# Optimization experiments

Measured on AMD Instinct MI355X. Metric: run time of the kernel, lower is better.

The kernel has to match this reference:

```python
import jax, jax.numpy as jnp
import numpy as np

# wav2vec2 feature-extractor conv stack config: (kernel, stride) per layer, 512 channels
CONV_CFG = [(10, 5), (3, 2), (3, 2), (3, 2), (3, 2), (2, 2), (2, 2)]
C = 512
PROJ = 256
HID = 128
NCLS = 5
N_WORDS = 64
B = 8
L = 40000


def _conv1d(h, w, stride):
    # h: [B, Cin, T], w: [Cout, Cin, K]
    return jax.lax.conv_general_dilated(
        h, w, window_strides=(stride,), padding='VALID',
        dimension_numbers=('NCH', 'OIH', 'NCH'))


def setup_inputs() -> dict:
    key = jax.random.key(0)
    ks = jax.random.split(key, 16)
    x = jax.random.normal(ks[0], (B, L), dtype=jnp.float32)
    word_ids = jax.random.randint(ks[1], (B,), 0, N_WORDS)
    convs = {}
    cin = 1
    for i, (k, s) in enumerate(CONV_CFG):
        fan = cin * k
        convs[f'conv{i}'] = jax.random.normal(ks[2 + i], (C, cin, k), dtype=jnp.float32) / np.sqrt(fan)
        cin = C
    gn_scale = jnp.ones((C,), dtype=jnp.float32)
    gn_bias = jnp.zeros((C,), dtype=jnp.float32)
    proj_w = jax.random.normal(ks[9], (PROJ, C), dtype=jnp.float32) / np.sqrt(C)
    proj_b = jnp.zeros((PROJ,), dtype=jnp.float32)
    cls_w1 = jax.random.normal(ks[10], (N_WORDS, PROJ, HID), dtype=jnp.float32) / np.sqrt(PROJ)
    cls_b1 = jnp.zeros((N_WORDS, HID), dtype=jnp.float32)
    cls_w2 = jax.random.normal(ks[11], (N_WORDS, HID, NCLS), dtype=jnp.float32) / np.sqrt(HID)
    cls_b2 = jnp.zeros((N_WORDS, NCLS), dtype=jnp.float32)
    return dict(x=x, word_ids=word_ids, gn_scale=gn_scale, gn_bias=gn_bias,
                proj_w=proj_w, proj_b=proj_b, cls_w1=cls_w1, cls_b1=cls_b1,
                cls_w2=cls_w2, cls_b2=cls_b2, **convs)


def _forward(x, convs, gn_scale, gn_bias, proj_w, proj_b, cls_w1, cls_b1, cls_w2, cls_b2, word_ids):
    h = x[:, None, :]  # [B,1,L]
    for i, (k, s) in enumerate(CONV_CFG):
        h = _conv1d(h, convs[i], s)
        if i == 0:
            # wav2vec2 group-norm: groups == channels -> per-channel norm over time
            mu = jnp.mean(h, axis=-1, keepdims=True)
            var = jnp.var(h, axis=-1, keepdims=True)
            h = (h - mu) * jax.lax.rsqrt(var + 1e-5)
            h = h * gn_scale[None, :, None] + gn_bias[None, :, None]
        h = jax.nn.gelu(h)
    feat = jnp.mean(h, axis=-1)                          # [B, 512] mean-pool over time
    feat = jax.nn.relu(feat @ proj_w.T + proj_b)         # [B, 256] (dropout = identity in eval)
    w1 = cls_w1[word_ids]                                # [B, 256, 128] routed gather
    h1 = jax.nn.relu(jnp.einsum('bd,bdh->bh', feat, w1) + cls_b1[word_ids])
    out = jnp.einsum('bh,bho->bo', h1, cls_w2[word_ids]) + cls_b2[word_ids]  # [B, 5]
    return out


def reference(x, word_ids, gn_scale, gn_bias, proj_w, proj_b, cls_w1, cls_b1, cls_w2, cls_b2,
              conv0, conv1, conv2, conv3, conv4, conv5, conv6):
    convs = [conv0, conv1, conv2, conv3, conv4, conv5, conv6]
    return _forward(x, convs, gn_scale, gn_bias, proj_w, proj_b,
                    cls_w1, cls_b1, cls_w2, cls_b2, word_ids)
```

## Files before the change

kernel.cpp:

```cpp
#include <hip/hip_runtime.h>
#include <hip/hip_bf16.h>

typedef unsigned short u16;
typedef short bf16x8 __attribute__((ext_vector_type(8)));
typedef float f32x4 __attribute__((ext_vector_type(4)));

#define CC 512

constexpr int vmimm(int n) {
    return (n & 0xF) | ((n >> 4) << 14) | (0x7 << 4) | (0xF << 8);
}

__device__ __forceinline__ float gelu_tanh(float x) {
    float x3 = x * x * x;
    float z  = 0.7978845608028654f * (x + 0.044715f * x3);
    float e  = __expf(2.0f * z);
    float th = 1.0f - 2.0f / (e + 1.0f);
    return 0.5f * x * (1.0f + th);
}

__device__ __forceinline__ u16 f2bf(float f) {
    union { float f; unsigned u; } v; v.f = f;
    unsigned r = v.u + 0x7fff + ((v.u >> 16) & 1);
    return (u16)(r >> 16);
}
__device__ __forceinline__ float bf2f(u16 h) {
    union { unsigned u; float f; } v; v.u = ((unsigned)h) << 16; return v.f;
}

__global__ __launch_bounds__(256) void conv0_store(
    const float* __restrict__ x, const float* __restrict__ w0,
    u16* __restrict__ actG, float* __restrict__ part) {
    const int t0 = blockIdx.x * 64, b = blockIdx.y;
    __shared__ float xs[64 * 5 + 16];
    __shared__ float w0t[10 * 512];
    for (int i = threadIdx.x; i < 64 * 5 + 5; i += 256) {
        int gi = t0 * 5 + i;
        xs[i] = (gi < 40000) ? x[b * 40000 + gi] : 0.0f;
    }
    for (int i = threadIdx.x; i < 5120; i += 256) {
        int c = i / 10, j = i - c * 10;
        w0t[j * 512 + c] = w0[i];
    }
    __syncthreads();
    const int lane = threadIdx.x & 63, wv = threadIdx.x >> 6;
    float wr[8][10];
#pragma unroll
    for (int q = 0; q < 8; ++q)
#pragma unroll
        for (int j = 0; j < 10; ++j) wr[q][j] = w0t[j * 512 + lane + 64 * q];
    float sacc[8] = {}, qacc[8] = {};
    u16* ob = actG + ((size_t)b * 8320 + t0 + wv * 16) * 512 + lane;
#pragma unroll
    for (int u = 0; u < 16; ++u) {
        const int tt = wv * 16 + u;
        const int t  = t0 + tt;
        float xv[10];
#pragma unroll
        for (int j = 0; j < 10; ++j) xv[j] = xs[tt * 5 + j];
#pragma unroll
        for (int q = 0; q < 8; ++q) {
            float a = 0.0f;
#pragma unroll
            for (int j = 0; j < 10; ++j) a = fmaf(wr[q][j], xv[j], a);
            const u16 h = f2bf(a);
            ob[(size_t)u * 512 + 64 * q] = h;
            if (t < 7999) {
                const float ar = bf2f(h);
                sacc[q] += ar; qacc[q] += ar * ar;
            }
        }
    }
    float* pp = part + ((((size_t)blockIdx.x * 4 + wv) * 8 + b) * 512 + lane) * 2;
#pragma unroll
    for (int q = 0; q < 8; ++q) {
        pp[q * 128] = sacc[q]; pp[q * 128 + 1] = qacc[q];
    }
}

__global__ __launch_bounds__(256) void stats_finalizeAB(
    const float* __restrict__ part, const float* __restrict__ gsc,
    const float* __restrict__ gbi, float* __restrict__ Af, float* __restrict__ Bf) {
    const int row = blockIdx.x * 256 + threadIdx.x;
    float s = 0.0f, q = 0.0f;
    for (int k = 0; k < 500; ++k) {
        const float2 v = *(const float2*)(part + ((size_t)k * 4096 + row) * 2);
        s += v.x; q += v.y;
    }
    float mean = s / 7999.0f;
    float var  = fmaxf(q / 7999.0f - mean * mean, 0.0f);
    float rstd = rsqrtf(var + 1e-5f);
    const int c = row & (CC - 1);
    float A = rstd * gsc[c];
    Af[row] = A;
    Bf[row] = gbi[c] - mean * A;
}

__global__ __launch_bounds__(256) void gn_apply(
    u16* __restrict__ actG, const float* __restrict__ Af,
    const float* __restrict__ Bf) {
    const int b = blockIdx.y;
    const int idx = blockIdx.x * 256 + threadIdx.x;
    const int row = idx >> 6, c0 = (idx & 63) * 8;
    if (row >= 7999) return;
    u16* p = actG + ((size_t)b * 8320 + row) * 512 + c0;
    union { u16 s[8]; uint4 v; } in, outv;
    in.v = *(const uint4*)p;
    const float4 a0 = *(const float4*)(Af + b * 512 + c0);
    const float4 a1 = *(const float4*)(Af + b * 512 + c0 + 4);
    const float4 b0 = *(const float4*)(Bf + b * 512 + c0);
    const float4 b1 = *(const float4*)(Bf + b * 512 + c0 + 4);
    const float av[8] = {a0.x, a0.y, a0.z, a0.w, a1.x, a1.y, a1.z, a1.w};
    const float bv[8] = {b0.x, b0.y, b0.z, b0.w, b1.x, b1.y, b1.z, b1.w};
#pragma unroll
    for (int e = 0; e < 8; ++e)
        outv.s[e] = f2bf(gelu_tanh(fmaf(bf2f(in.s[e]), av[e], bv[e])));
    *(uint4*)p = outv.v;
}

template <int K, int NL>
struct WtBatch { const float* src[NL]; u16* dst[NL]; };

template <int K, int NL>
__global__ __launch_bounds__(256) void wt_transform(WtBatch<K, NL> a) {
    constexpr int WROW = 32 * K + 8;
    const int cit = blockIdx.x, cob = blockIdx.y, l = blockIdx.z;
    const float* w = a.src[l];
    u16* dst = a.dst[l] + ((size_t)(cob * 16 + cit)) * 128 * WROW;
    for (int idx = threadIdx.x; idx < 128 * WROW; idx += 256) {
        const int co = idx / WROW, e = idx - co * WROW;
        u16 hi = 0;
        if (e < 32 * K) {
            const int j = e >> 5, ci = e & 31;
            hi = f2bf(w[((size_t)(cob * 128 + co) * 512 + cit * 32 + ci) * K + j]);
        }
        dst[idx] = hi;
    }
}

template <int K, int TT>
__global__ __launch_bounds__(256, 2) void conv_mfma(
    const u16* __restrict__ act, int capIn,
    const u16* __restrict__ wt,
    u16* __restrict__ outAct, int capOut, int tbShift) {
    constexpr int WROW = 32 * K + 8;
    constexpr int XH   = TT + 8;
    constexpr int TF   = TT / 32;
    constexpr int TXC  = XH * 8;
    constexpr int CPX  = TXC / 4;
    constexpr int NIX  = (CPX + 63) / 64;
    constexpr int XLAST = CPX - (NIX - 1) * 64;
    constexpr int TWC  = 128 * WROW / 8;
    constexpr int CPW  = TWC / 4;
    constexpr int NIW  = (CPW + 63) / 64;
    constexpr int WLAST = CPW - (NIW - 1) * 64;

    __shared__ __align__(16) u16 Xs[2][XH * 64];
    __shared__ __align__(16) u16 Ws[128 * WROW];

    const int tid  = threadIdx.x;
    const int lane = tid & 63;
    const int wv   = tid >> 6;
    const int wco  = wv >> 1, wtt = wv & 1;
    const int l15  = lane & 15, l16 = lane >> 4;

    const int flat = blockIdx.x;
    const int xcd  = flat & 7, cob = (flat >> 3) & 3;
    const int G    = xcd + (flat >> 5) * 8;
    const int t_b  = G & ((1 << tbShift) - 1);
    const int b    = G >> tbShift;
    const int t0   = t_b * TT;
    const int x0   = t0 * 2;

    const char* abase = (const char*)(act + (size_t)b * capIn * 512);
    const u16*  wbase = wt + (size_t)cob * (16 * 128 * WROW);

    const char* xsA[NIX]; const char* xsB[NIX]; int xdst[NIX];
#pragma unroll
    for (int i = 0; i < NIX; ++i) {
        const int c  = wv * CPX + i * 64 + lane;
        const int xh = c >> 3;
        const int li = ((c & 7) * 16) ^ ((xh & 7) << 4);
        const int xx = min(x0 + 2 * xh + (li >> 6), capIn - 1);
        xsA[i] = abase + (size_t)xx * 1024 + (li & 63);
        xsB[i] = xsA[i] + 64;
        xdst[i] = (wv * CPX + i * 64) * 16;
    }
    const char* wsrc[NIW]; int wdst[NIW];
#pragma unroll
    for (int i = 0; i < NIW; ++i) {
        wsrc[i] = (const char*)wbase + (size_t)(wv * CPW + i * 64 + lane) * 16;
        wdst[i] = (wv * CPW + i * 64) * 16;
    }

    auto stageX = [&](const char* (&xs)[NIX], u16* xb) {
#pragma unroll
        for (int i = 0; i < NIX; ++i)
            if (i < NIX - 1 || lane < XLAST)
                __builtin_amdgcn_global_load_lds(
                    (const __attribute__((address_space(1))) void*)xs[i],
                    (__attribute__((address_space(3))) void*)((char*)xb + xdst[i]),
                    16, 0, 0);
#pragma unroll
        for (int i = 0; i < NIX; ++i) xs[i] += 128;
    };
    auto stageW = [&]() {
#pragma unroll
        for (int i = 0; i < NIW; ++i)
            if (i < NIW - 1 || lane < WLAST)
                __builtin_amdgcn_global_load_lds(
                    (const __attribute__((address_space(1))) void*)wsrc[i],
                    (__attribute__((address_space(3))) void*)((char*)&Ws[0] + wdst[i]),
                    16, 0, 0);
#pragma unroll
        for (int i = 0; i < NIW; ++i) wsrc[i] += WROW * 256;
    };

    int xoff[K][TF];
    int woff[K][4];
#pragma unroll
    for (int j = 0; j < K; ++j) {
#pragma unroll
        for (int tf = 0; tf < TF; ++tf) {
            const int tl = wtt * (TT / 2) + tf * 16 + l15;
            const int xl = 2 * tl + j;
            const int xh = xl >> 1, p = xl & 1;
            xoff[j][tf] = xh * 128 + ((p * 64 + l16 * 16) ^ ((xh & 7) << 4));
        }
#pragma unroll
        for (int cf = 0; cf < 4; ++cf)
            woff[j][cf] = ((wco * 64 + cf * 16 + l15) * WROW + j * 32 + l16 * 8) * 2;
    }

    f32x4 acc[4][TF] = {};

    stageX(xsA, &Xs[0][0]);
    stageX(xsB, &Xs[1][0]);
    stageW();
    __syncthreads();

    auto body = [&](int cit, u16* xb, const char* (&xset)[NIX]) {
        bf16x8 xr[K][TF], wr[K][4];
#pragma unroll
        for (int j = 0; j < K; ++j) {
#pragma unroll
            for (int tf = 0; tf < TF; ++tf)
                xr[j][tf] = *(const bf16x8*)((const char*)xb + xoff[j][tf]);
#pragma unroll
            for (int cf = 0; cf < 4; ++cf)
                wr[j][cf] = *(const bf16x8*)((const char*)&Ws[0] + woff[j][cf]);
        }
        asm volatile("s_waitcnt lgkmcnt(0)" ::: "memory");
        __builtin_amdgcn_s_barrier();
        if (cit < 15) stageW();
        if (cit < 14) stageX(xset, xb);
#pragma unroll
        for (int j = 0; j < K; ++j)
#pragma unroll
            for (int cf = 0; cf < 4; ++cf)
#pragma unroll
                for (int tf = 0; tf < TF; ++tf)
                    acc[cf][tf] = __builtin_amdgcn_mfma_f32_16x16x32_bf16(
                        wr[j][cf], xr[j][tf], acc[cf][tf], 0, 0, 0);
        if (cit < 14) {
            __builtin_amdgcn_s_waitcnt(vmimm(NIX));
            __builtin_amdgcn_s_barrier();
        } else if (cit == 14) {
            __builtin_amdgcn_s_waitcnt(vmimm(0));
            __builtin_amdgcn_s_barrier();
        }
    };

#pragma unroll 1
    for (int c2 = 0; c2 < 16; c2 += 2) {
        body(c2,     &Xs[0][0], xsA);
        body(c2 + 1, &Xs[1][0], xsB);
    }

    u16* ob = outAct + (size_t)b * capOut * 512;
#pragma unroll
    for (int cf = 0; cf < 4; ++cf) {
#pragma unroll
        for (int tf = 0; tf < TF; ++tf) {
            const int tG  = t0 + wtt * (TT / 2) + tf * 16 + l15;
            const int coG = cob * 128 + wco * 64 + cf * 16 + l16 * 4;
            union { u16 s[4]; uint2 v; } pk;
#pragma unroll
            for (int r = 0; r < 4; ++r)
                pk.s[r] = f2bf(gelu_tanh(acc[cf][tf][r]));
            *(uint2*)(ob + (size_t)tG * 512 + coG) = pk.v;
        }
    }
}

__global__ __launch_bounds__(512) void feat_proj_kernel(
    const u16* __restrict__ act, int cap,
    const float* __restrict__ pw, const float* __restrict__ pb,
    float* __restrict__ pfeat) {
    const int b = blockIdx.x;
    __shared__ float fs[8][512];
    __shared__ float feat[CC];
    const int c8 = (threadIdx.x & 63) * 8;
    const int tg = threadIdx.x >> 6;
    float s[8] = {};
    for (int t = tg; t < 124; t += 8) {
        union { u16 u[8]; uint4 v; } in;
        in.v = *(const uint4*)(act + ((size_t)b * cap + t) * 512 + c8);
#pragma unroll
        for (int e = 0; e < 8; ++e) s[e] += bf2f(in.u[e]);
    }
#pragma unroll
    for (int e = 0; e < 8; ++e) fs[tg][c8 + e] = s[e];
    __syncthreads();
    {
        const int c = threadIdx.x;
        if (c < 512) {
            float acc = 0.0f;
#pragma unroll
            for (int g = 0; g < 8; ++g) acc += fs[g][c];
            feat[c] = acc * (1.0f / 124.0f);
        }
    }
    __syncthreads();
    if (threadIdx.x < 256) {
        const int j = threadIdx.x;
        const float* wr = pw + (size_t)j * CC;
        float acc = pb[j];
        for (int cc = 0; cc < CC; ++cc) acc = fmaf(feat[cc], wr[cc], acc);
        pfeat[b * 256 + j] = fmaxf(acc, 0.0f);
    }
}

__global__ __launch_bounds__(128) void cls_kernel(
    const float* __restrict__ pfeat, const int* __restrict__ wid,
    const float* __restrict__ w1, const float* __restrict__ b1,
    const float* __restrict__ w2, const float* __restrict__ b2,
    float* __restrict__ out) {
    const int b = blockIdx.x;
    const int id = wid[b];
    __shared__ float pf[256], h1[128];
    for (int d = threadIdx.x; d < 256; d += 128) pf[d] = pfeat[b * 256 + d];
    __syncthreads();
    {
        const int hh = threadIdx.x;
        const float* w1p = w1 + (size_t)id * 256 * 128;
        float s = b1[id * 128 + hh];
        for (int d = 0; d < 256; ++d) s = fmaf(pf[d], w1p[d * 128 + hh], s);
        h1[hh] = fmaxf(s, 0.0f);
    }
    __syncthreads();
    if (threadIdx.x < 5) {
        const float* w2p = w2 + (size_t)id * 128 * 5;
        float s = b2[id * 5 + threadIdx.x];
        for (int hh = 0; hh < 128; ++hh) s = fmaf(h1[hh], w2p[hh * 5 + threadIdx.x], s);
        out[b * 5 + threadIdx.x] = s;
    }
}

extern "C" void kernel_launch(void* const* d_in, const int* in_sizes, int n_in,
                              void* d_out, int out_size, void* d_ws, size_t ws_size,
                              hipStream_t stream) {
    const float* x   = (const float*)d_in[0];
    const int*   wid = (const int*)d_in[1];
    const float* gsc = (const float*)d_in[2];
    const float* gbi = (const float*)d_in[3];
    const float* pw  = (const float*)d_in[4];
    const float* pb  = (const float*)d_in[5];
    const float* w1  = (const float*)d_in[6];
    const float* b1  = (const float*)d_in[7];
    const float* w2  = (const float*)d_in[8];
    const float* b2  = (const float*)d_in[9];
    const float* cw[7];
    for (int i = 0; i < 7; ++i) cw[i] = (const float*)d_in[10 + i];

    char* ws = (char*)d_ws;
    const size_t SZ_ACTG = (size_t)8 * 8320 * 512 * 2;
    const size_t SZ_P    = (size_t)8 * 4224 * 512 * 2;
    const size_t SZ_Q    = (size_t)8 * 2176 * 512 * 2;
    u16* actG = (u16*)ws;
    u16* bufP = (u16*)(ws + SZ_ACTG);
    u16* bufQ = (u16*)(ws + SZ_ACTG + SZ_P);
    size_t off = SZ_ACTG + SZ_P + SZ_Q;
    u16* wtbuf[7];
    for (int i = 1; i <= 4; ++i) { wtbuf[i] = (u16*)(ws + off); off += (size_t)4 * 16 * 128 * 104 * 2; }
    for (int i = 5; i <= 6; ++i) { wtbuf[i] = (u16*)(ws + off); off += (size_t)4 * 16 * 128 * 72 * 2; }
    off = (off + 255) & ~(size_t)255;
    float* statsPart = (float*)(ws + off); off += (size_t)500 * 8 * 512 * 2 * 4;
    float* Af        = (float*)(ws + off); off += 4096 * 4;
    float* Bf        = (float*)(ws + off); off += 4096 * 4;
    float* pfeat     = (float*)(ws + off); off += 8 * 256 * 4;

    conv0_store<<<dim3(125, 8), 256, 0, stream>>>(x, cw[0], actG, statsPart);
    stats_finalizeAB<<<dim3(16), 256, 0, stream>>>(statsPart, gsc, gbi, Af, Bf);
    gn_apply<<<dim3(2000, 8), 256, 0, stream>>>(actG, Af, Bf);

    {
        WtBatch<3, 4> a;
        for (int i = 0; i < 4; ++i) { a.src[i] = cw[1 + i]; a.dst[i] = wtbuf[1 + i]; }
        wt_transform<3, 4><<<dim3(16, 4, 4), 256, 0, stream>>>(a);
        WtBatch<2, 2> c;
        for (int i = 0; i < 2; ++i) { c.src[i] = cw[5 + i]; c.dst[i] = wtbuf[5 + i]; }
        wt_transform<2, 2><<<dim3(16, 4, 2), 256, 0, stream>>>(c);
    }

    conv_mfma<3, 128><<<dim3(32 * 32), 256, 0, stream>>>(actG, 8320, wtbuf[1], bufP, 4224, 5);
    conv_mfma<3, 128><<<dim3(16 * 32), 256, 0, stream>>>(bufP, 4224, wtbuf[2], bufQ, 2176, 4);
    conv_mfma<3,  64><<<dim3(16 * 32), 256, 0, stream>>>(bufQ, 2176, wtbuf[3], bufP, 4224, 4);
    conv_mfma<3,  64><<<dim3( 8 * 32), 256, 0, stream>>>(bufP, 4224, wtbuf[4], bufQ, 2176, 3);
    conv_mfma<2,  64><<<dim3( 4 * 32), 256, 0, stream>>>(bufQ, 2176, wtbuf[5], bufP, 4224, 2);
    conv_mfma<2,  64><<<dim3( 2 * 32), 256, 0, stream>>>(bufP, 4224, wtbuf[6], bufQ, 2176, 1);

    feat_proj_kernel<<<dim3(8), 512, 0, stream>>>(bufQ, 2176, pw, pb, pfeat);
    cls_kernel<<<dim3(8), 128, 0, stream>>>(pfeat, wid, w1, b1, w2, b2, (float*)d_out);
}
```

Before: 315.6 us.

## Recompute conv0 in a fused norm+GELU pass instead of storing and re-reading

The first conv layer is now computed twice: one pass only accumulates per-channel statistics, and a second pass recomputes the conv and applies group-norm and GELU before writing bf16 activations. This removes one write and one read-modify-write of the large layer-0 activation buffer in exchange for recomputing the cheap 10-tap conv. Padding rows past the valid length are now written as zero. The MFMA inner loop is also wrapped in s_setprio raise/lower to favour the matrix-issuing waves.

```diff
diff --git a/kernel.cpp b/kernel.cpp
--- a/kernel.cpp
+++ b/kernel.cpp
@@ -28,9 +28,9 @@
     union { unsigned u; float f; } v; v.u = ((unsigned)h) << 16; return v.f;
 }
 
-__global__ __launch_bounds__(256) void conv0_store(
+__global__ __launch_bounds__(256) void conv0_stats(
     const float* __restrict__ x, const float* __restrict__ w0,
-    u16* __restrict__ actG, float* __restrict__ part) {
+    float* __restrict__ part) {
     const int t0 = blockIdx.x * 64, b = blockIdx.y;
     __shared__ float xs[64 * 5 + 16];
     __shared__ float w0t[10 * 512];
@@ -50,7 +50,6 @@
 #pragma unroll
         for (int j = 0; j < 10; ++j) wr[q][j] = w0t[j * 512 + lane + 64 * q];
     float sacc[8] = {}, qacc[8] = {};
-    u16* ob = actG + ((size_t)b * 8320 + t0 + wv * 16) * 512 + lane;
 #pragma unroll
     for (int u = 0; u < 16; ++u) {
         const int tt = wv * 16 + u;
@@ -63,10 +62,8 @@
             float a = 0.0f;
 #pragma unroll
             for (int j = 0; j < 10; ++j) a = fmaf(wr[q][j], xv[j], a);
-            const u16 h = f2bf(a);
-            ob[(size_t)u * 512 + 64 * q] = h;
             if (t < 7999) {
-                const float ar = bf2f(h);
+                const float ar = bf2f(f2bf(a));
                 sacc[q] += ar; qacc[q] += ar * ar;
             }
         }
@@ -96,26 +93,54 @@
     Bf[row] = gbi[c] - mean * A;
 }
 
-__global__ __launch_bounds__(256) void gn_apply(
-    u16* __restrict__ actG, const float* __restrict__ Af,
-    const float* __restrict__ Bf) {
-    const int b = blockIdx.y;
-    const int idx = blockIdx.x * 256 + threadIdx.x;
-    const int row = idx >> 6, c0 = (idx & 63) * 8;
-    if (row >= 7999) return;
-    u16* p = actG + ((size_t)b * 8320 + row) * 512 + c0;
-    union { u16 s[8]; uint4 v; } in, outv;
-    in.v = *(const uint4*)p;
-    const float4 a0 = *(const float4*)(Af + b * 512 + c0);
-    const float4 a1 = *(const float4*)(Af + b * 512 + c0 + 4);
-    const float4 b0 = *(const float4*)(Bf + b * 512 + c0);
-    const float4 b1 = *(const float4*)(Bf + b * 512 + c0 + 4);
-    const float av[8] = {a0.x, a0.y, a0.z, a0.w, a1.x, a1.y, a1.z, a1.w};
-    const float bv[8] = {b0.x, b0.y, b0.z, b0.w, b1.x, b1.y, b1.z, b1.w};
-#pragma unroll
-    for (int e = 0; e < 8; ++e)
-        outv.s[e] = f2bf(gelu_tanh(fmaf(bf2f(in.s[e]), av[e], bv[e])));
-    *(uint4*)p = outv.v;
+__global__ __launch_bounds__(256) void conv0_norm(
+    const float* __restrict__ x, const float* __restrict__ w0,
+    const float* __restrict__ Af, const float* __restrict__ Bf,
+    u16* __restrict__ actG) {
+    const int t0 = blockIdx.x * 64, b = blockIdx.y;
+    __shared__ float xs[64 * 5 + 16];
+    __shared__ float w0t[10 * 512];
+    for (int i = threadIdx.x; i < 64 * 5 + 5; i += 256) {
+        int gi = t0 * 5 + i;
+        xs[i] = (gi < 40000) ? x[b * 40000 + gi] : 0.0f;
+    }
+    for (int i = threadIdx.x; i < 5120; i += 256) {
+        int c = i / 10, j = i - c * 10;
+        w0t[j * 512 + c] = w0[i];
+    }
+    __syncthreads();
+    const int lane = threadIdx.x & 63, wv = threadIdx.x >> 6;
+    float wr[8][10];
+    float Ar[8], Br[8];
+#pragma unroll
+    for (int q = 0; q < 8; ++q) {
+        const int c = lane + 64 * q;
+#pragma unroll
+        for (int j = 0; j < 10; ++j) wr[q][j] = w0t[j * 512 + c];
+        Ar[q] = Af[b * 512 + c];
+        Br[q] = Bf[b * 512 + c];
+    }
+    u16* ob = actG + ((size_t)b * 8320 + t0 + wv * 16) * 512 + lane;
+#pragma unroll
+    for (int u = 0; u < 16; ++u) {
+        const int tt = wv * 16 + u;
+        const int t  = t0 + tt;
+        float xv[10];
+#pragma unroll
+        for (int j = 0; j < 10; ++j) xv[j] = xs[tt * 5 + j];
+#pragma unroll
+        for (int q = 0; q < 8; ++q) {
+            float a = 0.0f;
+#pragma unroll
+            for (int j = 0; j < 10; ++j) a = fmaf(wr[q][j], xv[j], a);
+            u16 outv = 0;
+            if (t < 7999) {
+                const float ar = bf2f(f2bf(a));
+                outv = f2bf(gelu_tanh(fmaf(ar, Ar[q], Br[q])));
+            }
+            ob[(size_t)u * 512 + 64 * q] = outv;
+        }
+    }
 }
 
 template <int K, int NL>
@@ -254,6 +279,7 @@
         __builtin_amdgcn_s_barrier();
         if (cit < 15) stageW();
         if (cit < 14) stageX(xset, xb);
+        __builtin_amdgcn_s_setprio(1);
 #pragma unroll
         for (int j = 0; j < K; ++j)
 #pragma unroll
@@ -262,6 +288,7 @@
                 for (int tf = 0; tf < TF; ++tf)
                     acc[cf][tf] = __builtin_amdgcn_mfma_f32_16x16x32_bf16(
                         wr[j][cf], xr[j][tf], acc[cf][tf], 0, 0, 0);
+        __builtin_amdgcn_s_setprio(0);
         if (cit < 14) {
             __builtin_amdgcn_s_waitcnt(vmimm(NIX));
             __builtin_amdgcn_s_barrier();
@@ -390,9 +417,9 @@
     float* Bf        = (float*)(ws + off); off += 4096 * 4;
     float* pfeat     = (float*)(ws + off); off += 8 * 256 * 4;
 
-    conv0_store<<<dim3(125, 8), 256, 0, stream>>>(x, cw[0], actG, statsPart);
+    conv0_stats<<<dim3(125, 8), 256, 0, stream>>>(x, cw[0], statsPart);
     stats_finalizeAB<<<dim3(16), 256, 0, stream>>>(statsPart, gsc, gbi, Af, Bf);
-    gn_apply<<<dim3(2000, 8), 256, 0, stream>>>(actG, Af, Bf);
+    conv0_norm<<<dim3(125, 8), 256, 0, stream>>>(x, cw[0], Af, Bf, actG);
 
     {
         WtBatch<3, 4> a;
```

After: 327.4 us. 3.7% more time.
